# Performance work log

Hardware: AMD Instinct MI355X
Metric: run time of the kernel (lower is better)

Reference implementation:

```python
import jax, jax.numpy as jnp
import numpy as np

N_NODES = 50000
N_EDGES = 800000
IN_DIM = 256
OUT_DIM = 256


def setup_inputs() -> dict:
    key = jax.random.key(0)
    k_feat, k_src, k_dst, k_w0, k_w1, k_b = jax.random.split(key, 6)
    feat = jax.random.normal(k_feat, (N_NODES, IN_DIM), dtype=jnp.float32)
    src = jax.random.randint(k_src, (N_EDGES,), 0, N_NODES, dtype=jnp.int64)
    dst = jax.random.randint(k_dst, (N_EDGES,), 0, N_NODES, dtype=jnp.int64)
    # GraphConv weights (Glorot-ish scale) and biases
    W0 = jax.random.normal(k_w0, (IN_DIM, OUT_DIM), dtype=jnp.float32) / np.sqrt(IN_DIM)
    W1 = jax.random.normal(k_w1, (OUT_DIM, OUT_DIM), dtype=jnp.float32) / np.sqrt(OUT_DIM)
    b0 = jnp.zeros((OUT_DIM,), dtype=jnp.float32)
    b1 = jnp.zeros((OUT_DIM,), dtype=jnp.float32)
    # single shared nn.PReLU parameter (torch default init 0.25)
    prelu_a = jnp.asarray(0.25, dtype=jnp.float32)
    return {"feat": feat, "src": src, "dst": dst,
            "W0": W0, "b0": b0, "W1": W1, "b1": b1, "prelu_a": prelu_a}


def _prelu(x, a):
    return jnp.where(x >= 0, x, a * x)


def reference(feat, src, dst, W0, b0, W1, b1, prelu_a):
    N = feat.shape[0]
    ones = jnp.ones((src.shape[0],), dtype=feat.dtype)
    out_deg = jnp.zeros((N,), dtype=feat.dtype).at[src].add(ones)
    in_deg = jnp.zeros((N,), dtype=feat.dtype).at[dst].add(ones)
    # DGL norm='both': clamp degrees to >=1 before rsqrt
    norm_s = jax.lax.rsqrt(jnp.maximum(out_deg, 1.0))[:, None]  # [N,1]
    norm_d = jax.lax.rsqrt(jnp.maximum(in_deg, 1.0))[:, None]   # [N,1]

    def graph_conv(h, W, b):
        # h' = D_in^{-1/2} A (D_out^{-1/2} h) W + b
        msg = (h * norm_s)[src]                                   # [E, d]
        agg = jax.ops.segment_sum(msg, dst, num_segments=N)       # [N, d]
        return (agg * norm_d) @ W + b

    h = _prelu(graph_conv(feat, W0, b0), prelu_a)
    hg = jnp.sum(h, axis=0, keepdims=True)                        # SumPooling [1, d]
    h = _prelu(graph_conv(h, W1, b1), prelu_a)
    hg = jnp.concatenate([hg, jnp.sum(h, axis=0, keepdims=True)], axis=-1)
    return (h, hg)
```

## Files before the change

### kernel.cpp

```cpp
#include <hip/hip_runtime.h>
#include <stdint.h>

#define NN 50000
#define NE 800000
#define DIM 256

#define HB 128
#define HT 512
#define HALF 25000
#define HWORDS 12500

#define NSLICE 4
#define SCH 64
#define NPB 32
#define ECH 1024

#define GR 64
#define GB ((NN + GR - 1) / GR)

#define SCB 49

typedef __bf16 bf16x8 __attribute__((ext_vector_type(8)));
typedef float f32x4 __attribute__((ext_vector_type(4)));
typedef float f32x2 __attribute__((ext_vector_type(2)));
typedef unsigned u32x4 __attribute__((ext_vector_type(4)));
typedef int i32x4 __attribute__((ext_vector_type(4)));

__device__ __forceinline__ unsigned short f2bf(float f) {
  union { float f; unsigned u; } v; v.f = f;
  unsigned r = v.u + 0x7fffu + ((v.u >> 16) & 1u);
  return (unsigned short)(r >> 16);
}

__global__ __launch_bounds__(HT) void hist_kernel(const int* __restrict__ src,
                                                  const int* __restrict__ dst,
                                                  unsigned* __restrict__ Hs,
                                                  unsigned* __restrict__ Hd) {
  __shared__ unsigned lds[HALF];
  const int tid = threadIdx.x;
  const int phase = blockIdx.x >> 7;
  const int b = blockIdx.x & (HB - 1);
  const int* arr = phase ? dst : src;
  unsigned* H = phase ? Hd : Hs;
  for (int w = tid; w < HALF; w += HT) lds[w] = 0u;
  __syncthreads();
  for (int e = b * HT + tid; e < NE; e += HB * HT) {
    unsigned n = (unsigned)arr[e];
    atomicAdd(&lds[n >> 1], 1u << ((n & 1) * 16));
  }
  __syncthreads();
  for (int w = tid; w < HALF; w += HT)
    H[(size_t)b * HALF + w] = lds[w];
}

__global__ void reduce_norm_kernel(const unsigned* __restrict__ Hs,
                                   const unsigned* __restrict__ Hd,
                                   unsigned* __restrict__ Pd,
                                   int* __restrict__ in_cnt,
                                   float* __restrict__ norm_s,
                                   float* __restrict__ norm_d,
                                   float* __restrict__ hg) {
  int w = blockIdx.x * blockDim.x + threadIdx.x;
  if (blockIdx.x == 0) {
    hg[threadIdx.x] = 0.f;
    hg[256 + threadIdx.x] = 0.f;
  }
  if (w >= 2 * HWORDS) return;
  unsigned ss = 0, dd = 0;
  for (int b = 0; b < HB; ++b) {
    Pd[(size_t)b * HALF + w] = dd;
    ss += Hs[(size_t)b * HALF + w];
    dd += Hd[(size_t)b * HALF + w];
  }
  int n0 = w * 2;
  unsigned s0 = ss & 0xffffu, s1 = ss >> 16;
  unsigned d0 = dd & 0xffffu, d1 = dd >> 16;
  in_cnt[n0] = (int)d0;
  in_cnt[n0 + 1] = (int)d1;
  norm_s[n0] = rsqrtf(fmaxf((float)s0, 1.0f));
  norm_s[n0 + 1] = rsqrtf(fmaxf((float)s1, 1.0f));
  norm_d[n0] = rsqrtf(fmaxf((float)d0, 1.0f));
  norm_d[n0 + 1] = rsqrtf(fmaxf((float)d1, 1.0f));
}

__global__ __launch_bounds__(256) void scan_part_kernel(const int* __restrict__ in_cnt,
                                                        int* __restrict__ csum) {
  __shared__ int ws[4];
  int i0 = blockIdx.x * 1024 + threadIdx.x * 4;
  int s = 0;
#pragma unroll
  for (int j = 0; j < 4; ++j) {
    int i = i0 + j;
    if (i < NN) s += in_cnt[i];
  }
  int lane = threadIdx.x & 63, wave = threadIdx.x >> 6;
#pragma unroll
  for (int off = 32; off; off >>= 1) s += __shfl_down(s, off, 64);
  if (lane == 0) ws[wave] = s;
  __syncthreads();
  if (threadIdx.x == 0) csum[blockIdx.x] = ws[0] + ws[1] + ws[2] + ws[3];
}

__global__ __launch_bounds__(64) void scan_mid_kernel(const int* __restrict__ csum,
                                                      int* __restrict__ coff,
                                                      int* __restrict__ row_ptr) {
  int lane = threadIdx.x;
  int v = (lane < SCB) ? csum[lane] : 0;
  int incl = v;
#pragma unroll
  for (int off = 1; off < 64; off <<= 1) {
    int t = __shfl_up(incl, off, 64);
    if (lane >= off) incl += t;
  }
  if (lane < SCB) coff[lane] = incl - v;
  if (lane == SCB - 1) row_ptr[NN] = incl;
}

__global__ __launch_bounds__(256) void scan_write_kernel(const int* __restrict__ in_cnt,
                                                         const int* __restrict__ coff,
                                                         int* __restrict__ row_ptr) {
  __shared__ int wsum[4];
  int tid = threadIdx.x, lane = tid & 63, wave = tid >> 6;
  int i0 = blockIdx.x * 1024 + tid * 4;
  int v[4];
#pragma unroll
  for (int j = 0; j < 4; ++j) {
    int i = i0 + j;
    v[j] = (i < NN) ? in_cnt[i] : 0;
  }
  int tsum = v[0] + v[1] + v[2] + v[3];
  int incl = tsum;
#pragma unroll
  for (int off = 1; off < 64; off <<= 1) {
    int t = __shfl_up(incl, off, 64);
    if (lane >= off) incl += t;
  }
  if (lane == 63) wsum[wave] = incl;
  __syncthreads();
  int woff = 0;
  for (int w = 0; w < wave; ++w) woff += wsum[w];
  int run = coff[blockIdx.x] + woff + (incl - tsum);
#pragma unroll
  for (int j = 0; j < 4; ++j) {
    int i = i0 + j;
    if (i < NN) row_ptr[i] = run;
    run += v[j];
  }
}

__global__ __launch_bounds__(HT) void fill_kernel(const int* __restrict__ src,
                                                  const int* __restrict__ dst,
                                                  const int* __restrict__ row_ptr,
                                                  const unsigned* __restrict__ Pd,
                                                  int* __restrict__ colx) {
  __shared__ unsigned lds[HALF];
  const int tid = threadIdx.x;
  const int b = blockIdx.x;
  for (int w = tid; w < HALF; w += HT) lds[w] = 0u;
  __syncthreads();
  for (int e = b * HT + tid; e < NE; e += HB * HT) {
    int n = dst[e];
    int sh = (n & 1) * 16;
    unsigned old = atomicAdd(&lds[n >> 1], 1u << sh);
    unsigned rank = (old >> sh) & 0xffffu;
    unsigned pref = (Pd[(size_t)b * HALF + (n >> 1)] >> sh) & 0xffffu;
    colx[row_ptr[n] + (int)pref + (int)rank] = src[e] << 7;
  }
}

__device__ __forceinline__ void swizzleW_body(const float* __restrict__ W,
                                              unsigned short* __restrict__ Wb, int idx) {
  int lane = idx & 63;
  int blk = idx >> 6;
  int kc = blk & 7, nt = blk >> 3;
  int kbase = kc * 32 + (lane >> 4) * 8;
  int col = nt * 16 + (lane & 15);
  ushort4 o0, o1;
  o0.x = f2bf(W[(size_t)(kbase + 0) * DIM + col]);
  o0.y = f2bf(W[(size_t)(kbase + 1) * DIM + col]);
  o0.z = f2bf(W[(size_t)(kbase + 2) * DIM + col]);
  o0.w = f2bf(W[(size_t)(kbase + 3) * DIM + col]);
  o1.x = f2bf(W[(size_t)(kbase + 4) * DIM + col]);
  o1.y = f2bf(W[(size_t)(kbase + 5) * DIM + col]);
  o1.z = f2bf(W[(size_t)(kbase + 6) * DIM + col]);
  o1.w = f2bf(W[(size_t)(kbase + 7) * DIM + col]);
  ((ushort4*)Wb)[idx * 2 + 0] = o0;
  ((ushort4*)Wb)[idx * 2 + 1] = o1;
}

__global__ void prep_kernel(const float* __restrict__ feat, const float* __restrict__ norm_s,
                            unsigned short* __restrict__ featb,
                            const float* __restrict__ W0, unsigned short* __restrict__ Wb0,
                            const float* __restrict__ W1, unsigned short* __restrict__ Wb1) {
  int blk = blockIdx.x;
  if (blk < 12500) {
    int i = blk * 256 + threadIdx.x;
    int node = i >> 6;
    int ch4 = i & 63;
    float s = norm_s[node];
    float4 v = ((const float4*)feat)[i];
    ushort4 o;
    o.x = f2bf(v.x * s); o.y = f2bf(v.y * s); o.z = f2bf(v.z * s); o.w = f2bf(v.w * s);
    int sl = ch4 >> 4;
    int w4 = ch4 & 15;
    ((ushort4*)featb)[(size_t)sl * (NN * 16) + (size_t)node * 16 + w4] = o;
  } else if (blk < 12532) {
    swizzleW_body(W0, Wb0, (blk - 12500) * 256 + threadIdx.x);
  } else {
    swizzleW_body(W1, Wb1, (blk - 12532) * 256 + threadIdx.x);
  }
}

__device__ __forceinline__ void acc_row(f32x2* a, u32x4 p) {
  f32x2 v0 = { __uint_as_float(p.x << 16), __uint_as_float(p.x & 0xffff0000u) };
  a[0] += v0;
  f32x2 v1 = { __uint_as_float(p.y << 16), __uint_as_float(p.y & 0xffff0000u) };
  a[1] += v1;
  f32x2 v2 = { __uint_as_float(p.z << 16), __uint_as_float(p.z & 0xffff0000u) };
  a[2] += v2;
  f32x2 v3 = { __uint_as_float(p.w << 16), __uint_as_float(p.w & 0xffff0000u) };
  a[3] += v3;
}

__global__ __launch_bounds__(256) void agg_kernel(const unsigned short* __restrict__ X,
                                                  unsigned short* __restrict__ agg,
                                                  const int* __restrict__ row_ptr,
                                                  const int* __restrict__ colx,
                                                  const float* __restrict__ norm_d) {
  __shared__ int ecol[ECH];
  const int s = blockIdx.x & (NSLICE - 1);
  const int nb = blockIdx.x >> 2;
  const int tid = threadIdx.x;
  const int grp = tid >> 3;
  const int cl = tid & 7;
  const int node = nb * NPB + grp;

  const int nfirst = nb * NPB;
  const int nlast = (nfirst + NPB < NN) ? (nfirst + NPB) : NN;
  const int estart = row_ptr[nfirst];
  const int eend = row_ptr[nlast];

  int e = 0, end = 0;
  if (node < NN) { e = row_ptr[node]; end = row_ptr[node + 1]; }

  const char* Xp = (const char*)(X + (size_t)s * (NN * SCH));
  const int lsub = cl * 16;

  f32x2 a[4];
#pragma unroll
  for (int j = 0; j < 4; ++j) a[j] = (f32x2){0.f, 0.f};

  const int base0 = estart & ~3;
  for (int base = base0; base < eend; base += ECH) {
    const int lim = (base + ECH < eend) ? (base + ECH) : eend;
    __syncthreads();
    for (int k = base + tid * 4; k < lim; k += 1024) {
      i32x4 v = __builtin_nontemporal_load((const i32x4*)(colx + k));
      *(i32x4*)&ecol[k - base] = v;
    }
    __syncthreads();
    const int hi = (end < lim) ? end : lim;
    for (; e + 8 <= hi; e += 8) {
      int o_[8];
#pragma unroll
      for (int j = 0; j < 8; ++j) o_[j] = ecol[e - base + j];
      u32x4 r_[8];
#pragma unroll
      for (int j = 0; j < 8; ++j)
        r_[j] = *(const u32x4*)(Xp + (size_t)(unsigned)(o_[j] | lsub));
#pragma unroll
      for (int j = 0; j < 8; ++j) acc_row(a, r_[j]);
    }
    if (e + 4 <= hi) {
      int o_[4];
#pragma unroll
      for (int j = 0; j < 4; ++j) o_[j] = ecol[e - base + j];
      u32x4 r_[4];
#pragma unroll
      for (int j = 0; j < 4; ++j)
        r_[j] = *(const u32x4*)(Xp + (size_t)(unsigned)(o_[j] | lsub));
#pragma unroll
      for (int j = 0; j < 4; ++j) acc_row(a, r_[j]);
      e += 4;
    }
    for (; e < hi; ++e) {
      int o0 = ecol[e - base];
      u32x4 r = *(const u32x4*)(Xp + (size_t)(unsigned)(o0 | lsub));
      acc_row(a, r);
    }
  }

  if (node < NN) {
    float nd = norm_d[node];
    u32x4 o;
    o.x = (unsigned)f2bf(a[0].x * nd) | ((unsigned)f2bf(a[0].y * nd) << 16);
    o.y = (unsigned)f2bf(a[1].x * nd) | ((unsigned)f2bf(a[1].y * nd) << 16);
    o.z = (unsigned)f2bf(a[2].x * nd) | ((unsigned)f2bf(a[2].y * nd) << 16);
    o.w = (unsigned)f2bf(a[3].x * nd) | ((unsigned)f2bf(a[3].y * nd) << 16);
    __builtin_nontemporal_store(o, (u32x4*)(agg + (size_t)node * DIM + (size_t)s * SCH + (size_t)cl * 8));
  }
}

#define LDSROW 264
#define FROW 260
__global__ __launch_bounds__(256) void gemm_mfma_kernel(const unsigned short* __restrict__ A,
                                                        const unsigned short* __restrict__ Wb,
                                                        const float* __restrict__ bias,
                                                        const float* __restrict__ prelu_a_ptr,
                                                        const float* __restrict__ norm_s,
                                                        float* __restrict__ C,
                                                        unsigned short* __restrict__ Cb,
                                                        float* __restrict__ hg_part) {
  __shared__ unsigned short As[GR * LDSROW];
  int tid = threadIdx.x;
  int r0 = blockIdx.x * GR;
#pragma unroll
  for (int p = 0; p < 8; ++p) {
    int idx = p * 256 + tid;
    int row = idx >> 5;
    int seg = idx & 31;
    int grow = r0 + row;
    ushort4 v0 = {0, 0, 0, 0}, v1 = {0, 0, 0, 0};
    if (grow < NN) {
      const ushort4* g = (const ushort4*)(A + (size_t)grow * DIM + seg * 8);
      v0 = g[0]; v1 = g[1];
    }
    *(ushort4*)(&As[row * LDSROW + seg * 8 + 0]) = v0;
    *(ushort4*)(&As[row * LDSROW + seg * 8 + 4]) = v1;
  }
  __syncthreads();

  int wave = tid >> 6, lane = tid & 63;
  int quad = lane >> 4, l16 = lane & 15;

  f32x4 acc[4][4];
#pragma unroll
  for (int mt = 0; mt < 4; ++mt)
#pragma unroll
    for (int nti = 0; nti < 4; ++nti)
      acc[mt][nti] = (f32x4){0.f, 0.f, 0.f, 0.f};

#pragma unroll
  for (int kc = 0; kc < 8; ++kc) {
    bf16x8 a[4], b[4];
#pragma unroll
    for (int mt = 0; mt < 4; ++mt)
      a[mt] = *(const bf16x8*)(&As[(mt * 16 + l16) * LDSROW + kc * 32 + quad * 8]);
#pragma unroll
    for (int nti = 0; nti < 4; ++nti) {
      int nt = wave * 4 + nti;
      b[nti] = *(const bf16x8*)(Wb + ((size_t)(nt * 8 + kc) * 64 + lane) * 8);
    }
#pragma unroll
    for (int mt = 0; mt < 4; ++mt)
#pragma unroll
      for (int nti = 0; nti < 4; ++nti)
        acc[mt][nti] = __builtin_amdgcn_mfma_f32_16x16x32_bf16(a[mt], b[nti], acc[mt][nti], 0, 0, 0);
  }

  float pa = *prelu_a_ptr;
  float bv[4], cs[4];
#pragma unroll
  for (int nti = 0; nti < 4; ++nti) {
    bv[nti] = bias[wave * 64 + nti * 16 + l16];
    cs[nti] = 0.f;
  }
#pragma unroll
  for (int mt = 0; mt < 4; ++mt) {
#pragma unroll
    for (int nti = 0; nti < 4; ++nti) {
#pragma unroll
      for (int r = 0; r < 4; ++r) {
        int rowg = r0 + mt * 16 + quad * 4 + r;
        float x = acc[mt][nti][r] + bv[nti];
        x = (x >= 0.f) ? x : pa * x;
        acc[mt][nti][r] = x;
        if (rowg < NN) cs[nti] += x;
      }
    }
  }
#pragma unroll
  for (int nti = 0; nti < 4; ++nti) {
    cs[nti] += __shfl_xor(cs[nti], 16, 64);
    cs[nti] += __shfl_xor(cs[nti], 32, 64);
  }
  if (quad == 0) {
#pragma unroll
    for (int nti = 0; nti < 4; ++nti)
      hg_part[(size_t)blockIdx.x * 256 + wave * 64 + nti * 16 + l16] = cs[nti];
  }

  float* LF = (float*)As;
#pragma unroll
  for (int chunk = 0; chunk < 4; ++chunk) {
    __syncthreads();
#pragma unroll
    for (int nti = 0; nti < 4; ++nti) {
      int colw = wave * 64 + nti * 16 + l16;
#pragma unroll
      for (int r = 0; r < 4; ++r)
        LF[(quad * 4 + r) * FROW + colw] = acc[chunk][nti][r];
    }
    __syncthreads();
    int rowbase = r0 + chunk * 16;
    if (C) {
#pragma unroll
      for (int s = 0; s < 4; ++s) {
        int g = s * 256 + tid;
        int row = g >> 6, cg = g & 63;
        int rowg = rowbase + row;
        if (rowg < NN) {
          float4 v = *(const float4*)&LF[row * FROW + cg * 4];
          *(float4*)(C + (size_t)rowg * DIM + cg * 4) = v;
        }
      }
    }
    if (Cb) {
#pragma unroll
      for (int s = 0; s < 2; ++s) {
        int g = s * 256 + tid;
        int row = g >> 5, cg = g & 31;
        int rowg = rowbase + row;
        if (rowg < NN) {
          float ns = norm_s[rowg];
          float4 v0 = *(const float4*)&LF[row * FROW + cg * 8];
          float4 v1 = *(const float4*)&LF[row * FROW + cg * 8 + 4];
          uint4 o;
          o.x = (unsigned)f2bf(v0.x * ns) | ((unsigned)f2bf(v0.y * ns) << 16);
          o.y = (unsigned)f2bf(v0.z * ns) | ((unsigned)f2bf(v0.w * ns) << 16);
          o.z = (unsigned)f2bf(v1.x * ns) | ((unsigned)f2bf(v1.y * ns) << 16);
          o.w = (unsigned)f2bf(v1.z * ns) | ((unsigned)f2bf(v1.w * ns) << 16);
          unsigned short* outp = Cb + (size_t)(cg >> 3) * (NN * SCH)
                               + (size_t)rowg * SCH + (size_t)(cg & 7) * 8;
          *(uint4*)outp = o;
        }
      }
    }
  }
}

__global__ __launch_bounds__(256) void hg_reduce_kernel(const float* __restrict__ hg_part,
                                                        float* __restrict__ hg) {
  const int layer = blockIdx.x >> 3;
  const int chunk = blockIdx.x & 7;
  const int c = threadIdx.x;
  const float* base = hg_part + (size_t)layer * GB * 256;
  const int per = (GB + 7) / 8;
  int b0 = chunk * per;
  int b1 = (b0 + per < GB) ? (b0 + per) : GB;
  float s0 = 0.f, s1 = 0.f, s2 = 0.f, s3 = 0.f;
  int b = b0;
  for (; b + 4 <= b1; b += 4) {
    s0 += base[(size_t)(b + 0) * 256 + c];
    s1 += base[(size_t)(b + 1) * 256 + c];
    s2 += base[(size_t)(b + 2) * 256 + c];
    s3 += base[(size_t)(b + 3) * 256 + c];
  }
  for (; b < b1; ++b) s0 += base[(size_t)b * 256 + c];
  atomicAdd(&hg[layer * 256 + c], (s0 + s1) + (s2 + s3));
}

extern "C" void kernel_launch(void* const* d_in, const int* in_sizes, int n_in,
                              void* d_out, int out_size, void* d_ws, size_t ws_size,
                              hipStream_t stream) {
  const float* feat = (const float*)d_in[0];
  const int* src    = (const int*)d_in[1];
  const int* dst    = (const int*)d_in[2];
  const float* W0   = (const float*)d_in[3];
  const float* b0   = (const float*)d_in[4];
  const float* W1   = (const float*)d_in[5];
  const float* b1   = (const float*)d_in[6];
  const float* pa   = (const float*)d_in[7];

  float* out_h = (float*)d_out;
  float* hg    = out_h + (size_t)NN * DIM;

  char* w = (char*)d_ws;
  int* in_cnt   = (int*)w;        w += (size_t)NN * 4;
  float* norm_s = (float*)w;      w += (size_t)NN * 4;
  float* norm_d = (float*)w;      w += (size_t)NN * 4;
  int* row_ptr  = (int*)w;        w += (size_t)(NN + 16) * 4;
  int* colx     = (int*)w;        w += (size_t)(NE + 4) * 4;
  int* csum     = (int*)w;        w += 64 * 4;
  int* coff     = (int*)w;        w += 64 * 4;
  unsigned short* Wb0 = (unsigned short*)w;  w += (size_t)DIM * DIM * 2;
  unsigned short* Wb1 = (unsigned short*)w;  w += (size_t)DIM * DIM * 2;
  float* hg_part = (float*)w;     w += (size_t)2 * GB * 256 * 4;
  uintptr_t ap = ((uintptr_t)w + 255) & ~(uintptr_t)255;
  unsigned short* featb = (unsigned short*)ap;
  unsigned short* aggb  = featb + (size_t)NN * DIM;
  unsigned* Hs = (unsigned*)featb;
  unsigned* Hd = Hs + (size_t)HB * HALF;
  unsigned* Pd = (unsigned*)aggb;

  const int agg_blocks = NSLICE * ((NN + NPB - 1) / NPB);

  hist_kernel<<<2 * HB, HT, 0, stream>>>(src, dst, Hs, Hd);
  reduce_norm_kernel<<<(2 * HWORDS + 255) / 256, 256, 0, stream>>>(Hs, Hd, Pd, in_cnt,
                                                                   norm_s, norm_d, hg);
  prep_kernel<<<12564, 256, 0, stream>>>(feat, norm_s, featb, W0, Wb0, W1, Wb1);
  scan_part_kernel<<<SCB, 256, 0, stream>>>(in_cnt, csum);
  scan_mid_kernel<<<1, 64, 0, stream>>>(csum, coff, row_ptr);
  scan_write_kernel<<<SCB, 256, 0, stream>>>(in_cnt, coff, row_ptr);
  fill_kernel<<<HB, HT, 0, stream>>>(src, dst, row_ptr, Pd, colx);

  agg_kernel<<<agg_blocks, 256, 0, stream>>>(featb, aggb, row_ptr, colx, norm_d);
  gemm_mfma_kernel<<<GB, 256, 0, stream>>>(aggb, Wb0, b0, pa, norm_s,
                                           (float*)nullptr, featb, hg_part);

  agg_kernel<<<agg_blocks, 256, 0, stream>>>(featb, aggb, row_ptr, colx, norm_d);
  gemm_mfma_kernel<<<GB, 256, 0, stream>>>(aggb, Wb1, b1, pa, norm_s,
                                           out_h, (unsigned short*)nullptr, hg_part + (size_t)GB * 256);

  hg_reduce_kernel<<<16, 256, 0, stream>>>(hg_part, hg);
}
```

Baseline: 314.2 us.

## Fuse degree scan partials into reduce kernel and swizzle agg layout for direct LDS loads

```diff
diff --git a/kernel.cpp b/kernel.cpp
--- a/kernel.cpp
+++ b/kernel.cpp
@@ -8,7 +8,6 @@
 #define HB 128
 #define HT 512
 #define HALF 25000
-#define HWORDS 12500
 
 #define NSLICE 4
 #define SCH 64
@@ -30,6 +29,12 @@
   union { float f; unsigned u; } v; v.f = f;
   unsigned r = v.u + 0x7fffu + ((v.u >> 16) & 1u);
   return (unsigned short)(r >> 16);
+}
+
+__device__ __forceinline__ void gload_lds16(const void* g, void* l) {
+  __builtin_amdgcn_global_load_lds(
+      (const __attribute__((address_space(1))) unsigned*)g,
+      (__attribute__((address_space(3))) unsigned*)l, 16, 0, 0);
 }
 
 __global__ __launch_bounds__(HT) void hist_kernel(const int* __restrict__ src,
@@ -53,74 +58,65 @@
     H[(size_t)b * HALF + w] = lds[w];
 }
 
-__global__ void reduce_norm_kernel(const unsigned* __restrict__ Hs,
-                                   const unsigned* __restrict__ Hd,
-                                   unsigned* __restrict__ Pd,
-                                   int* __restrict__ in_cnt,
-                                   float* __restrict__ norm_s,
-                                   float* __restrict__ norm_d,
-                                   float* __restrict__ hg) {
-  int w = blockIdx.x * blockDim.x + threadIdx.x;
-  if (blockIdx.x == 0) {
-    hg[threadIdx.x] = 0.f;
-    hg[256 + threadIdx.x] = 0.f;
-  }
-  if (w >= 2 * HWORDS) return;
+__global__ __launch_bounds__(512) void reduce_norm_kernel(const unsigned* __restrict__ Hs,
+                                                          const unsigned* __restrict__ Hd,
+                                                          unsigned* __restrict__ Pd,
+                                                          int* __restrict__ in_cnt,
+                                                          float* __restrict__ norm_s,
+                                                          float* __restrict__ norm_d,
+                                                          float* __restrict__ hg,
+                                                          int* __restrict__ csum) {
+  __shared__ int ws[8];
+  const int tid = threadIdx.x;
+  const int w = blockIdx.x * 512 + tid;
+  if (blockIdx.x == 0) hg[tid] = 0.f;
   unsigned ss = 0, dd = 0;
-  for (int b = 0; b < HB; ++b) {
-    Pd[(size_t)b * HALF + w] = dd;
-    ss += Hs[(size_t)b * HALF + w];
-    dd += Hd[(size_t)b * HALF + w];
-  }
-  int n0 = w * 2;
-  unsigned s0 = ss & 0xffffu, s1 = ss >> 16;
-  unsigned d0 = dd & 0xffffu, d1 = dd >> 16;
-  in_cnt[n0] = (int)d0;
-  in_cnt[n0 + 1] = (int)d1;
-  norm_s[n0] = rsqrtf(fmaxf((float)s0, 1.0f));
-  norm_s[n0 + 1] = rsqrtf(fmaxf((float)s1, 1.0f));
-  norm_d[n0] = rsqrtf(fmaxf((float)d0, 1.0f));
-  norm_d[n0 + 1] = rsqrtf(fmaxf((float)d1, 1.0f));
-}
-
-__global__ __launch_bounds__(256) void scan_part_kernel(const int* __restrict__ in_cnt,
-                                                        int* __restrict__ csum) {
-  __shared__ int ws[4];
-  int i0 = blockIdx.x * 1024 + threadIdx.x * 4;
-  int s = 0;
-#pragma unroll
-  for (int j = 0; j < 4; ++j) {
-    int i = i0 + j;
-    if (i < NN) s += in_cnt[i];
-  }
-  int lane = threadIdx.x & 63, wave = threadIdx.x >> 6;
-#pragma unroll
-  for (int off = 32; off; off >>= 1) s += __shfl_down(s, off, 64);
-  if (lane == 0) ws[wave] = s;
+  if (w < HALF) {
+    for (int b = 0; b < HB; ++b) {
+      Pd[(size_t)b * HALF + w] = dd;
+      ss += Hs[(size_t)b * HALF + w];
+      dd += Hd[(size_t)b * HALF + w];
+    }
+    int n0 = w * 2;
+    unsigned s0 = ss & 0xffffu, s1 = ss >> 16;
+    unsigned d0 = dd & 0xffffu, d1 = dd >> 16;
+    in_cnt[n0] = (int)d0;
+    in_cnt[n0 + 1] = (int)d1;
+    norm_s[n0] = rsqrtf(fmaxf((float)s0, 1.0f));
+    norm_s[n0 + 1] = rsqrtf(fmaxf((float)s1, 1.0f));
+    norm_d[n0] = rsqrtf(fmaxf((float)d0, 1.0f));
+    norm_d[n0 + 1] = rsqrtf(fmaxf((float)d1, 1.0f));
+  }
+  int deg = (int)((dd & 0xffffu) + (dd >> 16));
+  int lane = tid & 63, wave = tid >> 6;
+#pragma unroll
+  for (int off = 32; off; off >>= 1) deg += __shfl_down(deg, off, 64);
+  if (lane == 0) ws[wave] = deg;
   __syncthreads();
-  if (threadIdx.x == 0) csum[blockIdx.x] = ws[0] + ws[1] + ws[2] + ws[3];
-}
-
-__global__ __launch_bounds__(64) void scan_mid_kernel(const int* __restrict__ csum,
-                                                      int* __restrict__ coff,
-                                                      int* __restrict__ row_ptr) {
-  int lane = threadIdx.x;
-  int v = (lane < SCB) ? csum[lane] : 0;
-  int incl = v;
-#pragma unroll
-  for (int off = 1; off < 64; off <<= 1) {
-    int t = __shfl_up(incl, off, 64);
-    if (lane >= off) incl += t;
-  }
-  if (lane < SCB) coff[lane] = incl - v;
-  if (lane == SCB - 1) row_ptr[NN] = incl;
+  if (tid == 0) {
+    int s = 0;
+#pragma unroll
+    for (int i = 0; i < 8; ++i) s += ws[i];
+    csum[blockIdx.x] = s;
+  }
 }
 
 __global__ __launch_bounds__(256) void scan_write_kernel(const int* __restrict__ in_cnt,
-                                                         const int* __restrict__ coff,
+                                                         const int* __restrict__ csum,
                                                          int* __restrict__ row_ptr) {
   __shared__ int wsum[4];
   int tid = threadIdx.x, lane = tid & 63, wave = tid >> 6;
+  int cv = (lane < SCB) ? csum[lane] : 0;
+  int cincl = cv;
+#pragma unroll
+  for (int off = 1; off < 64; off <<= 1) {
+    int t = __shfl_up(cincl, off, 64);
+    if (lane >= off) cincl += t;
+  }
+  int myoff = __shfl(cincl, blockIdx.x, 64) - __shfl(cv, blockIdx.x, 64);
+  int total = __shfl(cincl, SCB - 1, 64);
+  if (blockIdx.x == 0 && tid == 0) row_ptr[NN] = total;
+
   int i0 = blockIdx.x * 1024 + tid * 4;
   int v[4];
 #pragma unroll
@@ -139,7 +135,7 @@
   __syncthreads();
   int woff = 0;
   for (int w = 0; w < wave; ++w) woff += wsum[w];
-  int run = coff[blockIdx.x] + woff + (incl - tsum);
+  int run = myoff + woff + (incl - tsum);
 #pragma unroll
   for (int j = 0; j < 4; ++j) {
     int i = i0 + j;
@@ -297,11 +293,11 @@
     o.y = (unsigned)f2bf(a[1].x * nd) | ((unsigned)f2bf(a[1].y * nd) << 16);
     o.z = (unsigned)f2bf(a[2].x * nd) | ((unsigned)f2bf(a[2].y * nd) << 16);
     o.w = (unsigned)f2bf(a[3].x * nd) | ((unsigned)f2bf(a[3].y * nd) << 16);
-    __builtin_nontemporal_store(o, (u32x4*)(agg + (size_t)node * DIM + (size_t)s * SCH + (size_t)cl * 8));
-  }
-}
-
-#define LDSROW 264
+    unsigned pcol = (unsigned)(s * 128 + cl * 16) ^ (((unsigned)node & 7u) << 4);
+    __builtin_nontemporal_store(o, (u32x4*)((char*)agg + (size_t)node * 512 + pcol));
+  }
+}
+
 #define FROW 260
 __global__ __launch_bounds__(256) void gemm_mfma_kernel(const unsigned short* __restrict__ A,
                                                         const unsigned short* __restrict__ Wb,
@@ -311,22 +307,18 @@
                                                         float* __restrict__ C,
                                                         unsigned short* __restrict__ Cb,
                                                         float* __restrict__ hg_part) {
-  __shared__ unsigned short As[GR * LDSROW];
+  __shared__ __attribute__((aligned(16))) char Asb[GR * 512];
   int tid = threadIdx.x;
   int r0 = blockIdx.x * GR;
+  const char* Ab = (const char*)A;
 #pragma unroll
   for (int p = 0; p < 8; ++p) {
-    int idx = p * 256 + tid;
-    int row = idx >> 5;
-    int seg = idx & 31;
+    int off = p * 4096 + tid * 16;
+    int row = off >> 9;
+    int col = off & 511;
     int grow = r0 + row;
-    ushort4 v0 = {0, 0, 0, 0}, v1 = {0, 0, 0, 0};
-    if (grow < NN) {
-      const ushort4* g = (const ushort4*)(A + (size_t)grow * DIM + seg * 8);
-      v0 = g[0]; v1 = g[1];
-    }
-    *(ushort4*)(&As[row * LDSROW + seg * 8 + 0]) = v0;
-    *(ushort4*)(&As[row * LDSROW + seg * 8 + 4]) = v1;
+    if (grow > NN - 1) grow = NN - 1;
+    gload_lds16(Ab + (size_t)grow * 512 + col, Asb + off);
   }
   __syncthreads();
 
@@ -344,8 +336,11 @@
   for (int kc = 0; kc < 8; ++kc) {
     bf16x8 a[4], b[4];
 #pragma unroll
-    for (int mt = 0; mt < 4; ++mt)
-      a[mt] = *(const bf16x8*)(&As[(mt * 16 + l16) * LDSROW + kc * 32 + quad * 8]);
+    for (int mt = 0; mt < 4; ++mt) {
+      int row = mt * 16 + l16;
+      int c = (kc * 64 + quad * 16) ^ ((row & 7) << 4);
+      a[mt] = *(const bf16x8*)(Asb + row * 512 + c);
+    }
 #pragma unroll
     for (int nti = 0; nti < 4; ++nti) {
       int nt = wave * 4 + nti;
@@ -390,7 +385,7 @@
       hg_part[(size_t)blockIdx.x * 256 + wave * 64 + nti * 16 + l16] = cs[nti];
   }
 
-  float* LF = (float*)As;
+  float* LF = (float*)Asb;
 #pragma unroll
   for (int chunk = 0; chunk < 4; ++chunk) {
     __syncthreads();
@@ -482,7 +477,6 @@
   int* row_ptr  = (int*)w;        w += (size_t)(NN + 16) * 4;
   int* colx     = (int*)w;        w += (size_t)(NE + 4) * 4;
   int* csum     = (int*)w;        w += 64 * 4;
-  int* coff     = (int*)w;        w += 64 * 4;
   unsigned short* Wb0 = (unsigned short*)w;  w += (size_t)DIM * DIM * 2;
   unsigned short* Wb1 = (unsigned short*)w;  w += (size_t)DIM * DIM * 2;
   float* hg_part = (float*)w;     w += (size_t)2 * GB * 256 * 4;
@@ -496,12 +490,9 @@
   const int agg_blocks = NSLICE * ((NN + NPB - 1) / NPB);
 
   hist_kernel<<<2 * HB, HT, 0, stream>>>(src, dst, Hs, Hd);
-  reduce_norm_kernel<<<(2 * HWORDS + 255) / 256, 256, 0, stream>>>(Hs, Hd, Pd, in_cnt,
-                                                                   norm_s, norm_d, hg);
+  reduce_norm_kernel<<<SCB, 512, 0, stream>>>(Hs, Hd, Pd, in_cnt, norm_s, norm_d, hg, csum);
   prep_kernel<<<12564, 256, 0, stream>>>(feat, norm_s, featb, W0, Wb0, W1, Wb1);
-  scan_part_kernel<<<SCB, 256, 0, stream>>>(in_cnt, csum);
-  scan_mid_kernel<<<1, 64, 0, stream>>>(csum, coff, row_ptr);
-  scan_write_kernel<<<SCB, 256, 0, stream>>>(in_cnt, coff, row_ptr);
+  scan_write_kernel<<<SCB, 256, 0, stream>>>(in_cnt, csum, row_ptr);
   fill_kernel<<<HB, HT, 0, stream>>>(src, dst, row_ptr, Pd, colx);
 
   agg_kernel<<<agg_blocks, 256, 0, stream>>>(featb, aggb, row_ptr, colx, norm_d);
```

Measured after the change: 303.3 us. 1.04x faster.
